# Optimization experiments

Hardware: AMD Instinct MI355X
Metric: run time of the kernel (lower is better)

Reference implementation:

```python
import jax, jax.numpy as jnp
import numpy as np

OUT, IN = 4096, 4096
B, S = 4, 2048


def setup_inputs() -> dict:
    key = jax.random.key(0)
    k_x, k_wh, k_wm, k_wl, k_r, k_s, k_b = jax.random.split(key, 7)
    x = jax.random.normal(k_x, (B, S, IN), dtype=jnp.float32)
    r = jax.random.uniform(k_r, (OUT, IN))
    high_mask = r < 0.2
    medium_mask = (r < 0.5) & ~high_mask
    weight_high = jax.random.normal(k_wh, (OUT, IN), dtype=jnp.float32) * 0.02 * high_mask
    weight_medium = (jax.random.normal(k_wm, (OUT, IN), dtype=jnp.float32) * 0.02 * medium_mask).astype(jnp.float16)
    weight_low = jax.random.randint(k_wl, (OUT, IN), -127, 128, dtype=jnp.int32)
    low_scale = jax.random.uniform(k_s, (1,), dtype=jnp.float32) * 0.001 + 1e-4
    bias = jax.random.normal(k_b, (OUT,), dtype=jnp.float32) * 0.02
    return {
        "x": x,
        "weight_high": weight_high,
        "weight_medium": weight_medium,
        "weight_low": weight_low,
        "high_precision_mask": high_mask,
        "medium_precision_mask": medium_mask,
        "low_scale": low_scale,
        "bias": bias,
    }


def reference(x, weight_high, weight_medium, weight_low,
              high_precision_mask, medium_precision_mask, low_scale, bias):
    # Reconstruct full fp32 weight from three precision tiers (as in forward).
    low_mask = ~high_precision_mask & ~medium_precision_mask
    w = (weight_high
         + medium_precision_mask * weight_medium.astype(jnp.float32)
         + low_mask * (weight_low.astype(jnp.float32) * low_scale[0]))
    # F.linear: x @ w.T + bias ; [B,S,IN] x [OUT,IN] -> [B,S,OUT]
    return jnp.einsum('bsi,oi->bso', x, w) + bias
```

## Files before the change

kernel.cpp:

```cpp
#include <hip/hip_runtime.h>
#include <hip/hip_bf16.h>
#include <hip/hip_fp16.h>


#define M_DIM 8192
#define N_DIM 4096
#define K_DIM 4096

typedef __attribute__((ext_vector_type(8))) short short8;
typedef __attribute__((ext_vector_type(4))) float floatx4;
typedef __attribute__((ext_vector_type(8))) _Float16 half8;
typedef __attribute__((ext_vector_type(8))) unsigned char uchar8;
typedef __attribute__((ext_vector_type(4))) int intx4;

__device__ inline unsigned short f2bf(float f) {
    union { float f; unsigned u; } v; v.f = f;
    return (unsigned short)((v.u + 0x7fffu + ((v.u >> 16) & 1u)) >> 16);
}

__device__ inline void async16(const void* g, const void* l) {
    __builtin_amdgcn_global_load_lds(
        (const __attribute__((address_space(1))) void*)g,
        (__attribute__((address_space(3))) void*)l,
        16, 0, 0);
}

__global__ __launch_bounds__(256) void detect_kernel(const unsigned* __restrict__ wm_raw,
                                                     const unsigned* __restrict__ hm_raw,
                                                     int* __restrict__ flags) {
    __shared__ int s_f32cnt, s_maskbig;
    if (threadIdx.x == 0) { s_f32cnt = 0; s_maskbig = 0; }
    __syncthreads();
    union { unsigned u; float f; } w; w.u = wm_raw[threadIdx.x];
    float av = fabsf(w.f);
    if (av > 1e-4f && av < 1.0f) atomicAdd(&s_f32cnt, 1);
    if (hm_raw[threadIdx.x] > 1u) atomicAdd(&s_maskbig, 1);
    __syncthreads();
    if (threadIdx.x == 0) {
        flags[0] = (s_f32cnt >= 8) ? 1 : 0;
        flags[1] = (s_maskbig > 0) ? 1 : 0;
    }
}

__global__ __launch_bounds__(256) void cvt_x_kernel(const float* __restrict__ x,
                                                    unsigned short* __restrict__ o) {
    const int i = (blockIdx.x * 256 + threadIdx.x) * 8;
    floatx4 f0 = *(const floatx4*)(x + i);
    floatx4 f1 = *(const floatx4*)(x + i + 4);
    short8 s;
    s[0] = (short)f2bf(f0[0]); s[1] = (short)f2bf(f0[1]);
    s[2] = (short)f2bf(f0[2]); s[3] = (short)f2bf(f0[3]);
    s[4] = (short)f2bf(f1[0]); s[5] = (short)f2bf(f1[1]);
    s[6] = (short)f2bf(f1[2]); s[7] = (short)f2bf(f1[3]);
    *(short8*)(o + i) = s;
}

__global__ __launch_bounds__(256) void build_w_kernel(
        const float* __restrict__ wh, const void* __restrict__ wm_raw,
        const int* __restrict__ wl, const void* __restrict__ hm_raw,
        const void* __restrict__ mm_raw, const float* __restrict__ scale_p,
        const int* __restrict__ flags, unsigned short* __restrict__ o) {
    const int i = (blockIdx.x * 256 + threadIdx.x) * 8;
    const float scale = *scale_p;
    const bool wm_f32  = flags[0] != 0;
    const bool mask_u8 = flags[1] != 0;

    floatx4 h0 = *(const floatx4*)(wh + i);
    floatx4 h1 = *(const floatx4*)(wh + i + 4);
    intx4  l0 = *(const intx4*)(wl + i);
    intx4  l1 = *(const intx4*)(wl + i + 4);

    float mv[8];
    if (wm_f32) {
        floatx4 m0 = *(const floatx4*)((const float*)wm_raw + i);
        floatx4 m1 = *(const floatx4*)((const float*)wm_raw + i + 4);
#pragma unroll
        for (int e = 0; e < 4; ++e) { mv[e] = m0[e]; mv[e + 4] = m1[e]; }
    } else {
        half8 m = *(const half8*)((const _Float16*)wm_raw + i);
#pragma unroll
        for (int e = 0; e < 8; ++e) mv[e] = (float)m[e];
    }

    int lowmask[8];
    if (mask_u8) {
        uchar8 a = *(const uchar8*)((const unsigned char*)hm_raw + i);
        uchar8 b = *(const uchar8*)((const unsigned char*)mm_raw + i);
#pragma unroll
        for (int e = 0; e < 8; ++e) lowmask[e] = (a[e] | b[e]) == 0;
    } else {
        intx4 a0 = *(const intx4*)((const int*)hm_raw + i);
        intx4 a1 = *(const intx4*)((const int*)hm_raw + i + 4);
        intx4 b0 = *(const intx4*)((const int*)mm_raw + i);
        intx4 b1 = *(const intx4*)((const int*)mm_raw + i + 4);
#pragma unroll
        for (int e = 0; e < 4; ++e) {
            lowmask[e]     = (a0[e] | b0[e]) == 0;
            lowmask[e + 4] = (a1[e] | b1[e]) == 0;
        }
    }

    short8 s;
#pragma unroll
    for (int e = 0; e < 8; ++e) {
        float v = (e < 4 ? h0[e] : h1[e - 4]) + mv[e];
        int   lw = (e < 4 ? l0[e] : l1[e - 4]);
        if (lowmask[e]) v += (float)lw * scale;
        s[e] = (short)f2bf(v);
    }
    *(short8*)(o + i) = s;
}

__global__ __launch_bounds__(512, 2) void gemm256_kernel(
        const unsigned short* __restrict__ A,
        const unsigned short* __restrict__ Bw,
        const float* __restrict__ bias,
        float* __restrict__ out) {
    extern __shared__ char smem[];
    const int tid  = threadIdx.x;
    const int wave = tid >> 6, lane = tid & 63;
    const int lrow = lane & 15, lquad = lane >> 4;

    const int wg  = blockIdx.x;
    const int swz = (wg & 7) * 64 + (wg >> 3);
    const int bm0 = (swz >> 4) * 256;
    const int bn0 = (swz & 15) * 256;

    const int wr = wave >> 2, wc = wave & 3;
    const int wm = wr * 128, wn = wc * 64;

    const int lane2 = lane ^ ((lane & 32) ? 2 : 0);
    const int srow  = wave * 16 + (lane2 >> 2);
    const int scol  = (lane2 & 3) * 8;
    const unsigned short* gA0 = A  + (size_t)(bm0 + srow) * K_DIM + scol;
    const unsigned short* gA1 = gA0 + (size_t)128 * K_DIM;
    const unsigned short* gB0 = Bw + (size_t)(bn0 + srow) * K_DIM + scol;
    const unsigned short* gB1 = gB0 + (size_t)128 * K_DIM;
    const int dstA = wave * 1024;
    unsigned ko = 0;

    int offA[8], offB[4];
#pragma unroll
    for (int i = 0; i < 8; ++i) {
        int q = (wm + i * 16 + lrow) * 64 + lquad * 16;
        offA[i] = q ^ (((q >> 9) & 1) << 5);
    }
#pragma unroll
    for (int j = 0; j < 4; ++j) {
        int q = (wn + j * 16 + lrow) * 64 + lquad * 16;
        offB[j] = 16384 + (q ^ (((q >> 9) & 1) << 5));
    }

    floatx4 acc[8][4] = {};

#define STAGE(buf) do { \
        char* d_ = smem + (buf) * 32768 + dstA; \
        async16(gA0 + ko, d_); \
        async16(gA1 + ko, d_ + 8192); \
        async16(gB0 + ko, d_ + 16384); \
        async16(gB1 + ko, d_ + 24576); \
        ko += 32; } while (0)

#define COMPUTE(buf) do { \
        const char* ab_ = smem + (buf) * 32768; \
        short8 af[8], bq[4]; \
        _Pragma("unroll") \
        for (int i = 0; i < 8; ++i) af[i] = *(const short8*)(ab_ + offA[i]); \
        _Pragma("unroll") \
        for (int j = 0; j < 4; ++j) bq[j] = *(const short8*)(ab_ + offB[j]); \
        __builtin_amdgcn_s_setprio(1); \
        _Pragma("unroll") \
        for (int i = 0; i < 8; ++i) \
            _Pragma("unroll") \
            for (int j = 0; j < 4; ++j) \
                acc[i][j] = __builtin_amdgcn_mfma_f32_16x16x32_bf16(af[i], bq[j], acc[i][j], 0, 0, 0); \
        __builtin_amdgcn_s_setprio(0); } while (0)

#define WAITV(n) asm volatile("s_waitcnt vmcnt(" #n ")" ::: "memory")
#define BAR() do { __builtin_amdgcn_s_barrier(); asm volatile("" ::: "memory"); } while (0)

    STAGE(0); STAGE(1); STAGE(2);

    const int NT = K_DIM / 32;
    for (int t = 0; t < NT - 3; ++t) {
        WAITV(8);
        BAR();
        STAGE((t + 3) & 3);
        COMPUTE(t & 3);
    }
    WAITV(8); BAR(); COMPUTE((NT - 3) & 3);
    WAITV(4); BAR(); COMPUTE((NT - 2) & 3);
    WAITV(0); BAR(); COMPUTE((NT - 1) & 3);

#undef STAGE
#undef COMPUTE
#undef WAITV
#undef BAR

#pragma unroll
    for (int j = 0; j < 4; ++j) {
        const int col = bn0 + wn + j * 16 + lrow;
        const float bv = bias[col];
#pragma unroll
        for (int i = 0; i < 8; ++i) {
            const int row = bm0 + wm + i * 16 + lquad * 4;
#pragma unroll
            for (int r = 0; r < 4; ++r)
                out[(size_t)(row + r) * N_DIM + col] = acc[i][j][r] + bv;
        }
    }
}

__global__ __launch_bounds__(256) void gemm_fused_kernel(
        const float* __restrict__ X,
        const unsigned short* __restrict__ Bw,
        const float* __restrict__ bias,
        float* __restrict__ out) {
    __shared__ unsigned short As[128 * 32];
    __shared__ unsigned short Bs[128 * 32];
    const int tid  = threadIdx.x;
    const int wave = tid >> 6, lane = tid & 63;
    const int bm0 = blockIdx.y * 128, bn0 = blockIdx.x * 128;
    const int wm = (wave >> 1) * 64, wn = (wave & 1) * 64;
    const int lrow = lane & 15, lquad = lane >> 4;
    const int arow = tid >> 1, acol = (tid & 1) * 16;

    floatx4 acc[4][4] = {};

    for (int k0 = 0; k0 < K_DIM; k0 += 32) {
        __syncthreads();
#pragma unroll
        for (int c = 0; c < 2; ++c) {
            const int lb  = wave * 2048 + c * 1024;
            const int e   = (lb >> 1) + lane * 8;
            const int row = e >> 5, col = e & 31;
            async16(Bw + (size_t)(bn0 + row) * K_DIM + k0 + col, (const char*)Bs + lb);
        }
        {
            const float* g = X + (size_t)(bm0 + arow) * K_DIM + k0 + acol;
            floatx4 f0 = *(const floatx4*)(g);
            floatx4 f1 = *(const floatx4*)(g + 4);
            floatx4 f2 = *(const floatx4*)(g + 8);
            floatx4 f3 = *(const floatx4*)(g + 12);
            short8 s0, s1;
            s0[0]=(short)f2bf(f0[0]); s0[1]=(short)f2bf(f0[1]); s0[2]=(short)f2bf(f0[2]); s0[3]=(short)f2bf(f0[3]);
            s0[4]=(short)f2bf(f1[0]); s0[5]=(short)f2bf(f1[1]); s0[6]=(short)f2bf(f1[2]); s0[7]=(short)f2bf(f1[3]);
            s1[0]=(short)f2bf(f2[0]); s1[1]=(short)f2bf(f2[1]); s1[2]=(short)f2bf(f2[2]); s1[3]=(short)f2bf(f2[3]);
            s1[4]=(short)f2bf(f3[0]); s1[5]=(short)f2bf(f3[1]); s1[6]=(short)f2bf(f3[2]); s1[7]=(short)f2bf(f3[3]);
            *(short8*)&As[arow * 32 + acol]     = s0;
            *(short8*)&As[arow * 32 + acol + 8] = s1;
        }
        __syncthreads();

        short8 af[4], bf[4];
#pragma unroll
        for (int i = 0; i < 4; ++i)
            af[i] = *(const short8*)&As[(wm + i * 16 + lrow) * 32 + lquad * 8];
#pragma unroll
        for (int j = 0; j < 4; ++j)
            bf[j] = *(const short8*)&Bs[(wn + j * 16 + lrow) * 32 + lquad * 8];
#pragma unroll
        for (int i = 0; i < 4; ++i)
#pragma unroll
            for (int j = 0; j < 4; ++j)
                acc[i][j] = __builtin_amdgcn_mfma_f32_16x16x32_bf16(af[i], bf[j], acc[i][j], 0, 0, 0);
    }

#pragma unroll
    for (int j = 0; j < 4; ++j) {
        const int col = bn0 + wn + j * 16 + lrow;
        const float bv = bias[col];
#pragma unroll
        for (int i = 0; i < 4; ++i) {
            const int row = bm0 + wm + i * 16 + lquad * 4;
#pragma unroll
            for (int r = 0; r < 4; ++r)
                out[(size_t)(row + r) * N_DIM + col] = acc[i][j][r] + bv;
        }
    }
}

extern "C" void kernel_launch(void* const* d_in, const int* in_sizes, int n_in,
                              void* d_out, int out_size, void* d_ws, size_t ws_size,
                              hipStream_t stream) {
    const float*    x     = (const float*)d_in[0];
    const float*    wh    = (const float*)d_in[1];
    const void*     wmed  = d_in[2];
    const int*      wl    = (const int*)d_in[3];
    const void*     hm    = d_in[4];
    const void*     mm    = d_in[5];
    const float*    scale = (const float*)d_in[6];
    const float*    bias  = (const float*)d_in[7];
    float*          out   = (float*)d_out;

    int*            flags = (int*)d_ws;
    unsigned short* wbf   = (unsigned short*)((char*)d_ws + 256);
    unsigned short* xbf   = (unsigned short*)((char*)d_ws + 256 + (size_t)N_DIM * K_DIM * 2);
    const size_t need_full = 256 + (size_t)N_DIM * K_DIM * 2 + (size_t)M_DIM * K_DIM * 2;

    static bool attr_done = false;
    if (!attr_done) {
        (void)hipFuncSetAttribute(reinterpret_cast<const void*>(gemm256_kernel),
                                  hipFuncAttributeMaxDynamicSharedMemorySize, 131072);
        attr_done = true;
    }

    detect_kernel<<<1, 256, 0, stream>>>((const unsigned*)wmed, (const unsigned*)hm, flags);
    build_w_kernel<<<N_DIM * K_DIM / 2048, 256, 0, stream>>>(wh, wmed, wl, hm, mm, scale, flags, wbf);

    if (ws_size >= need_full) {
        cvt_x_kernel<<<M_DIM * K_DIM / 2048, 256, 0, stream>>>(x, xbf);
        gemm256_kernel<<<dim3(512), dim3(512), 131072, stream>>>(xbf, wbf, bias, out);
    } else {
        dim3 grid(N_DIM / 128, M_DIM / 128);
        gemm_fused_kernel<<<grid, 256, 0, stream>>>(x, wbf, bias, out);
    }
}
```

Before: 679.9 us.

## Fuse prep kernels and split GEMM main loop into interleaved half-tile phases

Measured after the change: 675.1 us. Within noise of the previous version (-0.7%).

```diff
diff --git a/kernel.cpp b/kernel.cpp
--- a/kernel.cpp
+++ b/kernel.cpp
@@ -25,45 +25,36 @@
         16, 0, 0);
 }
 
-__global__ __launch_bounds__(256) void detect_kernel(const unsigned* __restrict__ wm_raw,
-                                                     const unsigned* __restrict__ hm_raw,
-                                                     int* __restrict__ flags) {
-    __shared__ int s_f32cnt, s_maskbig;
-    if (threadIdx.x == 0) { s_f32cnt = 0; s_maskbig = 0; }
-    __syncthreads();
-    union { unsigned u; float f; } w; w.u = wm_raw[threadIdx.x];
-    float av = fabsf(w.f);
-    if (av > 1e-4f && av < 1.0f) atomicAdd(&s_f32cnt, 1);
-    if (hm_raw[threadIdx.x] > 1u) atomicAdd(&s_maskbig, 1);
-    __syncthreads();
-    if (threadIdx.x == 0) {
-        flags[0] = (s_f32cnt >= 8) ? 1 : 0;
-        flags[1] = (s_maskbig > 0) ? 1 : 0;
-    }
-}
-
-__global__ __launch_bounds__(256) void cvt_x_kernel(const float* __restrict__ x,
-                                                    unsigned short* __restrict__ o) {
-    const int i = (blockIdx.x * 256 + threadIdx.x) * 8;
-    floatx4 f0 = *(const floatx4*)(x + i);
-    floatx4 f1 = *(const floatx4*)(x + i + 4);
-    short8 s;
-    s[0] = (short)f2bf(f0[0]); s[1] = (short)f2bf(f0[1]);
-    s[2] = (short)f2bf(f0[2]); s[3] = (short)f2bf(f0[3]);
-    s[4] = (short)f2bf(f1[0]); s[5] = (short)f2bf(f1[1]);
-    s[6] = (short)f2bf(f1[2]); s[7] = (short)f2bf(f1[3]);
-    *(short8*)(o + i) = s;
-}
-
-__global__ __launch_bounds__(256) void build_w_kernel(
+__global__ __launch_bounds__(256) void prep_kernel(
+        const float* __restrict__ x,
         const float* __restrict__ wh, const void* __restrict__ wm_raw,
         const int* __restrict__ wl, const void* __restrict__ hm_raw,
         const void* __restrict__ mm_raw, const float* __restrict__ scale_p,
-        const int* __restrict__ flags, unsigned short* __restrict__ o) {
-    const int i = (blockIdx.x * 256 + threadIdx.x) * 8;
+        unsigned short* __restrict__ wbf, unsigned short* __restrict__ xbf) {
+    const int bid = blockIdx.x;
+    const int tid = threadIdx.x;
+
+    if (bid >= 8192) {
+        const size_t i = ((size_t)(bid - 8192) * 256 + tid) * 8;
+        floatx4 f0 = *(const floatx4*)(x + i);
+        floatx4 f1 = *(const floatx4*)(x + i + 4);
+        short8 s;
+        s[0] = (short)f2bf(f0[0]); s[1] = (short)f2bf(f0[1]);
+        s[2] = (short)f2bf(f0[2]); s[3] = (short)f2bf(f0[3]);
+        s[4] = (short)f2bf(f1[0]); s[5] = (short)f2bf(f1[1]);
+        s[6] = (short)f2bf(f1[2]); s[7] = (short)f2bf(f1[3]);
+        *(short8*)(xbf + i) = s;
+        return;
+    }
+
+    const int lane = tid & 63;
+    union { unsigned u; float f; } pw; pw.u = ((const unsigned*)wm_raw)[lane];
+    const float pav = fabsf(pw.f);
+    const bool wm_f32  = __popcll(__ballot(pav > 1e-4f && pav < 1.0f)) >= 4;
+    const bool mask_u8 = __ballot(((const unsigned*)hm_raw)[lane] > 1u) != 0;
+
+    const size_t i = ((size_t)bid * 256 + tid) * 8;
     const float scale = *scale_p;
-    const bool wm_f32  = flags[0] != 0;
-    const bool mask_u8 = flags[1] != 0;
 
     floatx4 h0 = *(const floatx4*)(wh + i);
     floatx4 h1 = *(const floatx4*)(wh + i + 4);
@@ -108,7 +99,7 @@
         if (lowmask[e]) v += (float)lw * scale;
         s[e] = (short)f2bf(v);
     }
-    *(short8*)(o + i) = s;
+    *(short8*)(wbf + i) = s;
 }
 
 __global__ __launch_bounds__(512, 2) void gemm256_kernel(
@@ -137,7 +128,6 @@
     const unsigned short* gB0 = Bw + (size_t)(bn0 + srow) * K_DIM + scol;
     const unsigned short* gB1 = gB0 + (size_t)128 * K_DIM;
     const int dstA = wave * 1024;
-    unsigned ko = 0;
 
     int offA[8], offB[4];
 #pragma unroll
@@ -153,49 +143,73 @@
 
     floatx4 acc[8][4] = {};
 
-#define STAGE(buf) do { \
-        char* d_ = smem + (buf) * 32768 + dstA; \
-        async16(gA0 + ko, d_); \
-        async16(gA1 + ko, d_ + 8192); \
-        async16(gB0 + ko, d_ + 16384); \
-        async16(gB1 + ko, d_ + 24576); \
-        ko += 32; } while (0)
-
-#define COMPUTE(buf) do { \
-        const char* ab_ = smem + (buf) * 32768; \
-        short8 af[8], bq[4]; \
-        _Pragma("unroll") \
-        for (int i = 0; i < 8; ++i) af[i] = *(const short8*)(ab_ + offA[i]); \
-        _Pragma("unroll") \
-        for (int j = 0; j < 4; ++j) bq[j] = *(const short8*)(ab_ + offB[j]); \
-        __builtin_amdgcn_s_setprio(1); \
-        _Pragma("unroll") \
-        for (int i = 0; i < 8; ++i) \
-            _Pragma("unroll") \
-            for (int j = 0; j < 4; ++j) \
-                acc[i][j] = __builtin_amdgcn_mfma_f32_16x16x32_bf16(af[i], bq[j], acc[i][j], 0, 0, 0); \
-        __builtin_amdgcn_s_setprio(0); } while (0)
+#define STAGEF(TILE) do { \
+        char* d_ = smem + ((TILE) & 3) * 32768 + dstA; \
+        const unsigned ko_ = (unsigned)(TILE) * 32u; \
+        async16(gA0 + ko_, d_); async16(gA1 + ko_, d_ + 8192); \
+        async16(gB0 + ko_, d_ + 16384); async16(gB1 + ko_, d_ + 24576); } while (0)
 
 #define WAITV(n) asm volatile("s_waitcnt vmcnt(" #n ")" ::: "memory")
 #define BAR() do { __builtin_amdgcn_s_barrier(); asm volatile("" ::: "memory"); } while (0)
-
-    STAGE(0); STAGE(1); STAGE(2);
+#define LGKM0() asm volatile("s_waitcnt lgkmcnt(0)" ::: "memory")
+#define SCHED0() __builtin_amdgcn_sched_barrier(0)
+
+#define PHASES(T, DO_STAGE) do { \
+        const char* ab_ = smem + ((T) & 3) * 32768; \
+        const unsigned ko3_ = ((unsigned)(T) + 3u) * 32u; \
+        short8 af_[4], bq_[4], ag_[4]; \
+        _Pragma("unroll") \
+        for (int i_ = 0; i_ < 4; ++i_) af_[i_] = *(const short8*)(ab_ + offA[i_]); \
+        _Pragma("unroll") \
+        for (int j_ = 0; j_ < 4; ++j_) bq_[j_] = *(const short8*)(ab_ + offB[j_]); \
+        if (DO_STAGE) { char* d_ = smem + (((T) + 3) & 3) * 32768 + dstA; \
+            async16(gA0 + ko3_, d_); async16(gA1 + ko3_, d_ + 8192); } \
+        SCHED0(); \
+        BAR(); \
+        LGKM0(); \
+        SCHED0(); \
+        __builtin_amdgcn_s_setprio(1); \
+        _Pragma("unroll") \
+        for (int i_ = 0; i_ < 4; ++i_) \
+            _Pragma("unroll") \
+            for (int j_ = 0; j_ < 4; ++j_) \
+                acc[i_][j_] = __builtin_amdgcn_mfma_f32_16x16x32_bf16(af_[i_], bq_[j_], acc[i_][j_], 0, 0, 0); \
+        __builtin_amdgcn_s_setprio(0); \
+        _Pragma("unroll") \
+        for (int i_ = 0; i_ < 4; ++i_) ag_[i_] = *(const short8*)(ab_ + offA[4 + i_]); \
+        if (DO_STAGE) { char* d_ = smem + (((T) + 3) & 3) * 32768 + dstA; \
+            async16(gB0 + ko3_, d_ + 16384); async16(gB1 + ko3_, d_ + 24576); } \
+        SCHED0(); \
+        BAR(); \
+        LGKM0(); \
+        SCHED0(); \
+        __builtin_amdgcn_s_setprio(1); \
+        _Pragma("unroll") \
+        for (int i_ = 0; i_ < 4; ++i_) \
+            _Pragma("unroll") \
+            for (int j_ = 0; j_ < 4; ++j_) \
+                acc[4 + i_][j_] = __builtin_amdgcn_mfma_f32_16x16x32_bf16(ag_[i_], bq_[j_], acc[4 + i_][j_], 0, 0, 0); \
+        __builtin_amdgcn_s_setprio(0); \
+    } while (0)
+
+    STAGEF(0); STAGEF(1); STAGEF(2);
 
     const int NT = K_DIM / 32;
     for (int t = 0; t < NT - 3; ++t) {
         WAITV(8);
         BAR();
-        STAGE((t + 3) & 3);
-        COMPUTE(t & 3);
-    }
-    WAITV(8); BAR(); COMPUTE((NT - 3) & 3);
-    WAITV(4); BAR(); COMPUTE((NT - 2) & 3);
-    WAITV(0); BAR(); COMPUTE((NT - 1) & 3);
-
-#undef STAGE
-#undef COMPUTE
+        PHASES(t, true);
+    }
+    WAITV(8); BAR(); PHASES(NT - 3, false);
+    WAITV(4); BAR(); PHASES(NT - 2, false);
+    WAITV(0); BAR(); PHASES(NT - 1, false);
+
+#undef STAGEF
+#undef PHASES
 #undef WAITV
 #undef BAR
+#undef LGKM0
+#undef SCHED0
 
 #pragma unroll
     for (int j = 0; j < 4; ++j) {
@@ -293,7 +307,6 @@
     const float*    bias  = (const float*)d_in[7];
     float*          out   = (float*)d_out;
 
-    int*            flags = (int*)d_ws;
     unsigned short* wbf   = (unsigned short*)((char*)d_ws + 256);
     unsigned short* xbf   = (unsigned short*)((char*)d_ws + 256 + (size_t)N_DIM * K_DIM * 2);
     const size_t need_full = 256 + (size_t)N_DIM * K_DIM * 2 + (size_t)M_DIM * K_DIM * 2;
@@ -305,13 +318,11 @@
         attr_done = true;
     }
 
-    detect_kernel<<<1, 256, 0, stream>>>((const unsigned*)wmed, (const unsigned*)hm, flags);
-    build_w_kernel<<<N_DIM * K_DIM / 2048, 256, 0, stream>>>(wh, wmed, wl, hm, mm, scale, flags, wbf);
-
     if (ws_size >= need_full) {
-        cvt_x_kernel<<<M_DIM * K_DIM / 2048, 256, 0, stream>>>(x, xbf);
+        prep_kernel<<<24576, 256, 0, stream>>>(x, wh, wmed, wl, hm, mm, scale, wbf, xbf);
         gemm256_kernel<<<dim3(512), dim3(512), 131072, stream>>>(xbf, wbf, bias, out);
     } else {
+        prep_kernel<<<8192, 256, 0, stream>>>(x, wh, wmed, wl, hm, mm, scale, wbf, wbf);
         dim3 grid(N_DIM / 128, M_DIM / 128);
         gemm_fused_kernel<<<grid, 256, 0, stream>>>(x, wbf, bias, out);
     }
```
